# Performance work log

Hardware: AMD Instinct MI355X
Metric: run time of the kernel (lower is better)

## Reference

```python
import jax, jax.numpy as jnp
import numpy as np

S, B, IN, HID, DEPTH = 512, 64, 512, 512, 5
KEEP_IN = 1.0 - 0.75   # input_dropout = 0.75
KEEP_HID = 1.0 - 0.25  # hidden_dropout = 0.25


def _lin_init(k, shape, fan_in):
    bound = 1.0 / np.sqrt(fan_in)
    return jax.random.uniform(k, shape, jnp.float32, -bound, bound)


def setup_inputs() -> dict:
    key = jax.random.key(0)
    ks = jax.random.split(key, 14)
    inp = jax.random.normal(ks[0], (S, B, IN), jnp.float32)
    hidden = jax.random.normal(ks[1], (B, HID), jnp.float32)
    # tied_noise=True -> one input mask shared by H/T/C, one hidden mask shared
    h_mask = jax.random.bernoulli(ks[2], KEEP_IN, (B, IN)).astype(jnp.float32) / KEEP_IN
    s_h_mask = jax.random.bernoulli(ks[3], KEEP_HID, (B, HID)).astype(jnp.float32) / KEEP_HID
    # input projections (torch nn.Linear: W [out,in], y = x W^T + b)
    Wih = _lin_init(ks[4], (HID, IN), IN)
    bih = _lin_init(ks[5], (HID,), IN)
    Wit = _lin_init(ks[6], (HID, IN), IN)
    bit = _lin_init(ks[7], (HID,), IN)
    Wic = _lin_init(ks[8], (HID, IN), IN)
    bic = _lin_init(ks[9], (HID,), IN)
    # recurrent depth layers; layer 0 has no bias (set to 0)
    Wh = _lin_init(ks[10], (DEPTH, HID, HID), HID)
    bh = _lin_init(ks[11], (DEPTH, HID), HID).at[0].set(0.0)
    Wt = _lin_init(ks[12], (DEPTH, HID, HID), HID)
    bt = _lin_init(ks[13], (DEPTH, HID), HID).at[0].set(0.0)
    return dict(inp=inp, hidden=hidden, h_mask=h_mask, s_h_mask=s_h_mask,
                Wih=Wih, bih=bih, Wit=Wit, bit=bit, Wic=Wic, bic=bic,
                Wh=Wh, bh=bh, Wt=Wt, bt=bt)


def reference(inp, hidden, h_mask, s_h_mask, Wih, bih, Wit, bit, Wic, bic, Wh, bh, Wt, bt):
    # masked input (tied noise: same mask for H/T/C)
    mx = h_mask[None, :, :] * inp                      # [S,B,IN]
    H = jnp.einsum('sbi,hi->sbh', mx, Wih) + bih       # [S,B,HID]
    T = jnp.einsum('sbi,hi->sbh', mx, Wit) + bit
    C = jnp.einsum('sbi,hi->sbh', mx, Wic) + bic

    def step(s, htc):
        H_t, T_t, C_t = htc
        for l in range(DEPTH):
            sm = s_h_mask * s                          # [B,HID]
            lin_h = sm @ Wh[l].T + bh[l]
            lin_t = sm @ Wt[l].T + bt[l]               # NOTE: original uses rnn_t for C gate too
            if l == 0:
                h = jnp.tanh(H_t + lin_h)
                t = jax.nn.sigmoid(T_t + lin_t)
                c = jax.nn.sigmoid(C_t + lin_t)
            else:
                h = jnp.tanh(lin_h)
                t = jax.nn.sigmoid(lin_t)
                c = jax.nn.sigmoid(lin_t)
            s = h * t + s * c
        return s, s

    last, outs = jax.lax.scan(step, hidden, (H, T, C))
    return outs, last
```

## Files before the change

### kernel.cpp

```cpp
#include <hip/hip_runtime.h>
#include <math.h>

#define S_LEN 512
#define BATCH 64
#define IN_DIM 512
#define HID 512
#define DEPTH 5
#define N3 1536

typedef float floatx4 __attribute__((ext_vector_type(4)));
typedef unsigned int uintx4 __attribute__((ext_vector_type(4)));

__global__ __launch_bounds__(256) void rhn_inproj(
    const float* __restrict__ inp, const float* __restrict__ h_mask,
    const float* __restrict__ Wih, const float* __restrict__ Wit,
    const float* __restrict__ Wic, const float* __restrict__ bih,
    const float* __restrict__ bit_, const float* __restrict__ bic,
    float* __restrict__ HTC)
{
    constexpr int BM = 128, BN = 128, BK = 16, LW = BM + 4;
    __shared__ float As[BK][LW];
    __shared__ float Bs[BK][LW];
    const int m0 = blockIdx.x * BM;
    const int n0 = blockIdx.y * BN;
    const int tid = threadIdx.x;
    const int lrow = tid & 127;
    const int lkq  = tid >> 7;
    const int tx = tid & 15, ty = tid >> 4;

    const float* Arow = inp + (size_t)(m0 + lrow) * 512;
    const float* Mrow = h_mask + (size_t)((m0 + lrow) & 63) * 512;
    const int n = n0 + lrow;
    const float* Wrow = (n < 512) ? (Wih + (size_t)n * 512)
                       : (n < 1024) ? (Wit + (size_t)(n - 512) * 512)
                                    : (Wic + (size_t)(n - 1024) * 512);

    float acc[8][8] = {};

    for (int k0 = 0; k0 < 512; k0 += BK) {
#pragma unroll
        for (int it = 0; it < 2; ++it) {
            int kq = lkq * 2 + it;
            float4 av = *(const float4*)(Arow + k0 + kq * 4);
            float4 mv = *(const float4*)(Mrow + k0 + kq * 4);
            float4 bv = *(const float4*)(Wrow + k0 + kq * 4);
            As[kq * 4 + 0][lrow] = av.x * mv.x;
            As[kq * 4 + 1][lrow] = av.y * mv.y;
            As[kq * 4 + 2][lrow] = av.z * mv.z;
            As[kq * 4 + 3][lrow] = av.w * mv.w;
            Bs[kq * 4 + 0][lrow] = bv.x;
            Bs[kq * 4 + 1][lrow] = bv.y;
            Bs[kq * 4 + 2][lrow] = bv.z;
            Bs[kq * 4 + 3][lrow] = bv.w;
        }
        __syncthreads();
#pragma unroll
        for (int kk = 0; kk < BK; ++kk) {
            float4 a0 = *(const float4*)&As[kk][ty * 8];
            float4 a1 = *(const float4*)&As[kk][ty * 8 + 4];
            float4 bv0 = *(const float4*)&Bs[kk][tx * 8];
            float4 bv1 = *(const float4*)&Bs[kk][tx * 8 + 4];
            float am[8] = {a0.x, a0.y, a0.z, a0.w, a1.x, a1.y, a1.z, a1.w};
            float bn[8] = {bv0.x, bv0.y, bv0.z, bv0.w, bv1.x, bv1.y, bv1.z, bv1.w};
#pragma unroll
            for (int i = 0; i < 8; ++i)
#pragma unroll
                for (int j = 0; j < 8; ++j)
                    acc[i][j] += am[i] * bn[j];
        }
        __syncthreads();
    }

    float bias[8];
#pragma unroll
    for (int j = 0; j < 8; ++j) {
        int nn = n0 + tx * 8 + j;
        bias[j] = (nn < 512) ? bih[nn] : (nn < 1024) ? bit_[nn - 512] : bic[nn - 1024];
    }
#pragma unroll
    for (int i = 0; i < 8; ++i) {
        int mm = m0 + ty * 8 + i;
        float4 o0, o1;
        o0.x = acc[i][0] + bias[0]; o0.y = acc[i][1] + bias[1];
        o0.z = acc[i][2] + bias[2]; o0.w = acc[i][3] + bias[3];
        o1.x = acc[i][4] + bias[4]; o1.y = acc[i][5] + bias[5];
        o1.z = acc[i][6] + bias[6]; o1.w = acc[i][7] + bias[7];
        *(float4*)(HTC + (size_t)mm * N3 + n0 + tx * 8)     = o0;
        *(float4*)(HTC + (size_t)mm * N3 + n0 + tx * 8 + 4) = o1;
    }
}

__device__ __forceinline__ float fast_sig(float x) {
    return __builtin_amdgcn_rcpf(1.f + __expf(-x));
}
__device__ __forceinline__ float fast_tanh(float x) {
    return 2.f * fast_sig(2.f * x) - 1.f;
}

__global__ __launch_bounds__(512, 2) void rhn_scan(
    const float* __restrict__ hidden,
    const float* __restrict__ s_h_mask,
    const float* __restrict__ Wh, const float* __restrict__ bh,
    const float* __restrict__ Wt, const float* __restrict__ bt,
    const float* __restrict__ HTC,
    float* __restrict__ exch,
    float* __restrict__ out)
{
    __shared__ float sm_s[8][HID];
    __shared__ float linT[16][8];

    const int tid  = threadIdx.x;
    const int lane = tid & 63;
    const int w    = tid >> 6;
    const int c    = lane & 3;
    const int kq   = (lane >> 2) & 15;
    const int gh   = w * 4 + c;
    const int g    = gh >> 4;
    const int hl   = gh & 15;

    const int hi = blockIdx.x >> 3;
    const int bi = blockIdx.x & 7;
    const int h0 = hi * 16, b0 = bi * 8;

    const int myb = ((kq & 1) << 2) | (kq & 2) | ((kq >> 2) & 1);
    const bool own = (g == 0) && (kq < 8);
    const bool lw  = (g == 1) && (kq < 8);

    const float* Wsrc = g ? Wt : Wh;
    float4 Wreg[DEPTH * 8];
#pragma unroll
    for (int l = 0; l < DEPTH; ++l)
#pragma unroll
        for (int j = 0; j < 8; ++j)
            Wreg[l * 8 + j] = *(const float4*)(Wsrc
                + ((size_t)l * HID + (h0 + hl)) * HID + (size_t)(j * 16 + kq) * 4);

    float biasr[DEPTH];
    const float* bsrc = g ? bt : bh;
#pragma unroll
    for (int l = 0; l < DEPTH; ++l) biasr[l] = bsrc[l * HID + h0 + hl];

    const int pA = tid,       pB = tid + 512;
    const int bA = pA >> 7,   kA = pA & 127;
    const int bB = pB >> 7,   kB = pB & 127;
    const size_t offA = ((size_t)(b0 + bA) * HID + (size_t)kA * 4) * sizeof(float);
    const size_t offB = ((size_t)(b0 + bB) * HID + (size_t)kB * 4) * sizeof(float);
    const size_t SLOT = (size_t)BATCH * HID * sizeof(float);

    float s = 0.f, mymask = 0.f, Hp = 0.f, Tp = 0.f, Cp = 0.f;
    size_t ownoff = 0;
    if (own) {
        const int gb = b0 + myb, hh = h0 + hl;
        s      = hidden[(size_t)gb * HID + hh];
        mymask = s_h_mask[(size_t)gb * HID + hh];
        const float* hp = HTC + (size_t)gb * N3 + hh;
        Hp = hp[0]; Tp = hp[512]; Cp = hp[1024];
        ownoff = ((size_t)gb * HID + hh) * sizeof(float);
        unsigned uu = (__float_as_uint(s * mymask) & ~7u);
        char* p = (char*)exch + ownoff;
        asm volatile("global_store_dword %0, %1, off sc1" :: "v"(p), "v"(uu) : "memory");
    }

    const float4* smq = (const float4*)&sm_s[0][0] + kq;

    int seq = 0;
    for (int step = 0; step < S_LEN; ++step) {
#define ROUND(L)                                                                  \
        {                                                                         \
            const unsigned tg = (unsigned)(seq & 7);                              \
            const char* sb = (const char*)exch + (size_t)(seq & 1) * SLOT;        \
            const char* pa = sb + offA;                                           \
            const char* pb = sb + offB;                                           \
            uintx4 ua, ub;                                                        \
            for (;;) {                                                            \
                asm volatile("global_load_dwordx4 %0, %2, off sc1\n\t"            \
                             "global_load_dwordx4 %1, %3, off sc1\n\t"            \
                             "s_waitcnt vmcnt(0)"                                 \
                             : "=&v"(ua), "=&v"(ub)                               \
                             : "v"(pa), "v"(pb) : "memory");                      \
                unsigned mm = (ua.x ^ tg) | (ua.y ^ tg) | (ua.z ^ tg) | (ua.w ^ tg) \
                            | (ub.x ^ tg) | (ub.y ^ tg) | (ub.z ^ tg) | (ub.w ^ tg); \
                if ((mm & 7u) == 0u) break;                                       \
            }                                                                     \
            *(uintx4*)&sm_s[bA][kA * 4] = ua;                                     \
            *(uintx4*)&sm_s[bB][kB * 4] = ub;                                     \
            __syncthreads();                         \
            float acc[8] = {0.f, 0.f, 0.f, 0.f, 0.f, 0.f, 0.f, 0.f};              \
            _Pragma("unroll")                                                     \
            for (int j = 0; j < 8; ++j) {                                         \
                const float4 wv = Wreg[(L) * 8 + j];                              \
                _Pragma("unroll")                                                 \
                for (int b = 0; b < 8; ++b) {                                     \
                    const float4 sv = smq[b * 128 + j * 16];                      \
                    acc[b] = fmaf(wv.x, sv.x, acc[b]);                            \
                    acc[b] = fmaf(wv.y, sv.y, acc[b]);                            \
                    acc[b] = fmaf(wv.z, sv.z, acc[b]);                            \
                    acc[b] = fmaf(wv.w, sv.w, acc[b]);                            \
                }                                                                 \
            }                                                                     \
            {           \
                const bool u0 = (lane & 4) != 0;                                  \
                const bool u1 = (lane & 8) != 0;                                  \
                const bool u2 = (lane & 16) != 0;                                 \
                _Pragma("unroll")                                                 \
                for (int i = 0; i < 4; ++i) {                                     \
                    float snd = u0 ? acc[i] : acc[i + 4];                         \
                    float kp  = u0 ? acc[i + 4] : acc[i];                         \
                    acc[i] = kp + __shfl_xor(snd, 4);                             \
                }                                                                 \
                _Pragma("unroll")                                                 \
                for (int i = 0; i < 2; ++i) {                                     \
                    float snd = u1 ? acc[i] : acc[i + 2];                         \
                    float kp  = u1 ? acc[i + 2] : acc[i];                         \
                    acc[i] = kp + __shfl_xor(snd, 8);                             \
                }                                                                 \
                {                                                                 \
                    float snd = u2 ? acc[0] : acc[1];                             \
                    float kp  = u2 ? acc[1] : acc[0];                             \
                    acc[0] = kp + __shfl_xor(snd, 16);                            \
                }                                                                 \
                acc[0] += __shfl_xor(acc[0], 32);                                 \
            }                                                                     \
            const float lin = acc[0] + biasr[L];                                  \
            if (lw) linT[hl][myb] = lin;                                          \
            __syncthreads();                \
            if (own) {                                                            \
                const float lt = linT[hl][myb];                                   \
                float hv, tv, cv;                                                 \
                if ((L) == 0) {                                                   \
                    hv = fast_tanh(Hp + lin);                                     \
                    tv = fast_sig(Tp + lt);                                       \
                    cv = fast_sig(Cp + lt);                                       \
                } else {                                                          \
                    hv = fast_tanh(lin);                                          \
                    tv = fast_sig(lt);                                            \
                    cv = tv;                                                      \
                }                                                                 \
                s = hv * tv + s * cv;                                             \
                unsigned uu = (__float_as_uint(s * mymask) & ~7u)                 \
                            | (unsigned)((seq + 1) & 7);                          \
                char* p = (char*)exch + (size_t)((seq + 1) & 1) * SLOT + ownoff;  \
                asm volatile("global_store_dword %0, %1, off sc1"                 \
                             :: "v"(p), "v"(uu) : "memory");                      \
                if ((L) == 0 && step + 1 < S_LEN) {                               \
                    const float* hp = HTC + ((size_t)(step + 1) * BATCH           \
                                      + (b0 + myb)) * N3 + (h0 + hl);             \
                    Hp = hp[0]; Tp = hp[512]; Cp = hp[1024];                      \
                }                                                                 \
                if ((L) == DEPTH - 1)                                             \
                    out[((size_t)step * BATCH + (b0 + myb)) * HID + (h0 + hl)] = s; \
            }                                                                     \
            ++seq;                                                                \
        }
        ROUND(0) ROUND(1) ROUND(2) ROUND(3) ROUND(4)
#undef ROUND
    }

    if (own)
        out[(size_t)S_LEN * BATCH * HID + (size_t)(b0 + myb) * HID + (h0 + hl)] = s;
}

extern "C" void kernel_launch(void* const* d_in, const int* in_sizes, int n_in,
                              void* d_out, int out_size, void* d_ws, size_t ws_size,
                              hipStream_t stream) {
    const float* inp      = (const float*)d_in[0];
    const float* hidden   = (const float*)d_in[1];
    const float* h_mask   = (const float*)d_in[2];
    const float* s_h_mask = (const float*)d_in[3];
    const float* Wih = (const float*)d_in[4];
    const float* bih = (const float*)d_in[5];
    const float* Wit = (const float*)d_in[6];
    const float* bit_ = (const float*)d_in[7];
    const float* Wic = (const float*)d_in[8];
    const float* bic = (const float*)d_in[9];
    const float* Wh = (const float*)d_in[10];
    const float* bh = (const float*)d_in[11];
    const float* Wt = (const float*)d_in[12];
    const float* bt = (const float*)d_in[13];
    float* out = (float*)d_out;

    float* HTC  = (float*)d_ws;
    float* exch = HTC + (size_t)32768 * N3;

    (void)hipMemsetAsync(exch, 0xFF, 2 * (size_t)BATCH * HID * sizeof(float), stream);

    dim3 g1(256, 12);
    rhn_inproj<<<g1, 256, 0, stream>>>(inp, h_mask, Wih, Wit, Wic, bih, bit_, bic, HTC);

    void* args[] = {(void*)&hidden, (void*)&s_h_mask, (void*)&Wh, (void*)&bh,
                    (void*)&Wt, (void*)&bt, (void*)&HTC, (void*)&exch, (void*)&out};
    (void)hipLaunchCooperativeKernel((void*)rhn_scan, dim3(256), dim3(512), args, 0, stream);
}
```

Baseline: 17.37 ms.

## Replace tagged-payload polling with per-wave flag counters for inter-block sync

Blocks stop encoding a 3-bit sequence tag in the low bits of each exchanged value. Each of the 4 owner waves now publishes a monotonically increasing counter flag after its stores drain. Readers spin on one flag dword before issuing a single payload load, instead of repeatedly reloading two dwordx4 payloads. This cuts polling traffic and keeps full-precision values, but adds a vmcnt wait plus a flag store per round and relies on store ordering between the payload and the flag.

```diff
diff --git a/kernel.cpp b/kernel.cpp
--- a/kernel.cpp
+++ b/kernel.cpp
@@ -104,6 +104,7 @@
     const float* __restrict__ Wt, const float* __restrict__ bt,
     const float* __restrict__ HTC,
     float* __restrict__ exch,
+    unsigned* __restrict__ flags,
     float* __restrict__ out)
 {
     __shared__ float sm_s[8][HID];
@@ -140,12 +141,14 @@
 #pragma unroll
     for (int l = 0; l < DEPTH; ++l) biasr[l] = bsrc[l * HID + h0 + hl];
 
-    const int pA = tid,       pB = tid + 512;
-    const int bA = pA >> 7,   kA = pA & 127;
-    const int bB = pB >> 7,   kB = pB & 127;
+    const int bA = tid >> 7,  kA = tid & 127;
+    const int bB = bA + 4,    kB = kA;
     const size_t offA = ((size_t)(b0 + bA) * HID + (size_t)kA * 4) * sizeof(float);
     const size_t offB = ((size_t)(b0 + bB) * HID + (size_t)kB * 4) * sizeof(float);
     const size_t SLOT = (size_t)BATCH * HID * sizeof(float);
+
+    const unsigned* fp = flags + (((size_t)bi * 32 + (kA >> 2)) * 4 + (kA & 3));
+    unsigned* fme = flags + (((size_t)bi * 32 + hi) * 4 + w);
 
     float s = 0.f, mymask = 0.f, Hp = 0.f, Tp = 0.f, Cp = 0.f;
     size_t ownoff = 0;
@@ -156,9 +159,17 @@
         const float* hp = HTC + (size_t)gb * N3 + hh;
         Hp = hp[0]; Tp = hp[512]; Cp = hp[1024];
         ownoff = ((size_t)gb * HID + hh) * sizeof(float);
-        unsigned uu = (__float_as_uint(s * mymask) & ~7u);
+        float v = s * mymask;
         char* p = (char*)exch + ownoff;
-        asm volatile("global_store_dword %0, %1, off sc1" :: "v"(p), "v"(uu) : "memory");
+        asm volatile("global_store_dword %0, %1, off sc1" :: "v"(p), "v"(v) : "memory");
+    }
+    if (w < 4) {
+        asm volatile("s_waitcnt vmcnt(0)" ::: "memory");
+        if (lane == 0) {
+            unsigned one = 1u;
+            asm volatile("global_store_dword %0, %1, off sc1"
+                         :: "v"(fme), "v"(one) : "memory");
+        }
     }
 
     const float4* smq = (const float4*)&sm_s[0][0] + kq;
@@ -167,21 +178,23 @@
     for (int step = 0; step < S_LEN; ++step) {
 #define ROUND(L)                                                                  \
         {                                                                         \
-            const unsigned tg = (unsigned)(seq & 7);                              \
+            const unsigned target = (unsigned)(seq + 1);                          \
             const char* sb = (const char*)exch + (size_t)(seq & 1) * SLOT;        \
             const char* pa = sb + offA;                                           \
             const char* pb = sb + offB;                                           \
+            unsigned fv;                                                          \
+            for (;;) {                                                            \
+                asm volatile("global_load_dword %0, %1, off sc1\n\t"              \
+                             "s_waitcnt vmcnt(0)"                                 \
+                             : "=v"(fv) : "v"(fp) : "memory");                    \
+                if (fv >= target) break;                                          \
+            }                                                                     \
             uintx4 ua, ub;                                                        \
-            for (;;) {                                                            \
-                asm volatile("global_load_dwordx4 %0, %2, off sc1\n\t"            \
-                             "global_load_dwordx4 %1, %3, off sc1\n\t"            \
-                             "s_waitcnt vmcnt(0)"                                 \
-                             : "=&v"(ua), "=&v"(ub)                               \
-                             : "v"(pa), "v"(pb) : "memory");                      \
-                unsigned mm = (ua.x ^ tg) | (ua.y ^ tg) | (ua.z ^ tg) | (ua.w ^ tg) \
-                            | (ub.x ^ tg) | (ub.y ^ tg) | (ub.z ^ tg) | (ub.w ^ tg); \
-                if ((mm & 7u) == 0u) break;                                       \
-            }                                                                     \
+            asm volatile("global_load_dwordx4 %0, %2, off sc1\n\t"                \
+                         "global_load_dwordx4 %1, %3, off sc1\n\t"                \
+                         "s_waitcnt vmcnt(0)"                                     \
+                         : "=&v"(ua), "=&v"(ub)                                   \
+                         : "v"(pa), "v"(pb) : "memory");                          \
             *(uintx4*)&sm_s[bA][kA * 4] = ua;                                     \
             *(uintx4*)&sm_s[bB][kB * 4] = ub;                                     \
             __syncthreads();                         \
@@ -237,18 +250,27 @@
                     cv = tv;                                                      \
                 }                                                                 \
                 s = hv * tv + s * cv;                                             \
-                unsigned uu = (__float_as_uint(s * mymask) & ~7u)                 \
-                            | (unsigned)((seq + 1) & 7);                          \
+                float v = s * mymask;                                             \
                 char* p = (char*)exch + (size_t)((seq + 1) & 1) * SLOT + ownoff;  \
                 asm volatile("global_store_dword %0, %1, off sc1"                 \
-                             :: "v"(p), "v"(uu) : "memory");                      \
+                             :: "v"(p), "v"(v) : "memory");                       \
+            }                                                                     \
+            if (w < 4) {      \
+                asm volatile("s_waitcnt vmcnt(0)" ::: "memory");                  \
+                if (lane == 0) {                                                  \
+                    unsigned nf = (unsigned)(seq + 2);                            \
+                    asm volatile("global_store_dword %0, %1, off sc1"             \
+                                 :: "v"(fme), "v"(nf) : "memory");                \
+                }                                                                 \
+            }                                                                     \
+            if (own) {           \
+                if ((L) == DEPTH - 1)                                             \
+                    out[((size_t)step * BATCH + (b0 + myb)) * HID + (h0 + hl)] = s; \
                 if ((L) == 0 && step + 1 < S_LEN) {                               \
                     const float* hp = HTC + ((size_t)(step + 1) * BATCH           \
                                       + (b0 + myb)) * N3 + (h0 + hl);             \
                     Hp = hp[0]; Tp = hp[512]; Cp = hp[1024];                      \
                 }                                                                 \
-                if ((L) == DEPTH - 1)                                             \
-                    out[((size_t)step * BATCH + (b0 + myb)) * HID + (h0 + hl)] = s; \
             }                                                                     \
             ++seq;                                                                \
         }
@@ -281,13 +303,15 @@
 
     float* HTC  = (float*)d_ws;
     float* exch = HTC + (size_t)32768 * N3;
-
-    (void)hipMemsetAsync(exch, 0xFF, 2 * (size_t)BATCH * HID * sizeof(float), stream);
+    unsigned* flags = (unsigned*)(exch + 2 * (size_t)BATCH * HID);
+
+    (void)hipMemsetAsync(flags, 0, 8 * 32 * 4 * sizeof(unsigned), stream);
 
     dim3 g1(256, 12);
     rhn_inproj<<<g1, 256, 0, stream>>>(inp, h_mask, Wih, Wit, Wic, bih, bit_, bic, HTC);
 
     void* args[] = {(void*)&hidden, (void*)&s_h_mask, (void*)&Wh, (void*)&bh,
-                    (void*)&Wt, (void*)&bt, (void*)&HTC, (void*)&exch, (void*)&out};
+                    (void*)&Wt, (void*)&bt, (void*)&HTC, (void*)&exch,
+                    (void*)&flags, (void*)&out};
     (void)hipLaunchCooperativeKernel((void*)rhn_scan, dim3(256), dim3(512), args, 0, stream);
 }
```

Result: slower. 25.87 ms (+48.9%).

## Add fast local-scope exchange buffer with fallback to system-coherent polling

Applied to the files above, without the earlier changes.

Each owner thread now writes its state to two exchange buffers: one stored with sc0 (narrower coherence scope) and one with sc1. Consumers first poll the sc0 copy a bounded number of times and switch permanently to the sc1 copy if the tagged values never appear. Polling loops gain s_sleep back-off and an iteration budget. The intent is cheaper cross-block handoff per depth round, at the cost of doubled stores and possible stale reads across XCDs, which would cause fallback or, once the budget runs out, silently wrong data.

```diff
diff --git a/kernel.cpp b/kernel.cpp
--- a/kernel.cpp
+++ b/kernel.cpp
@@ -7,6 +7,7 @@
 #define HID 512
 #define DEPTH 5
 #define N3 1536
+#define NBLK 256
 
 typedef float floatx4 __attribute__((ext_vector_type(4)));
 typedef unsigned int uintx4 __attribute__((ext_vector_type(4)));
@@ -103,7 +104,8 @@
     const float* __restrict__ Wh, const float* __restrict__ bh,
     const float* __restrict__ Wt, const float* __restrict__ bt,
     const float* __restrict__ HTC,
-    float* __restrict__ exch,
+    float* __restrict__ exch_g,
+    float* __restrict__ exch_l,
     float* __restrict__ out)
 {
     __shared__ float sm_s[8][HID];
@@ -140,9 +142,8 @@
 #pragma unroll
     for (int l = 0; l < DEPTH; ++l) biasr[l] = bsrc[l * HID + h0 + hl];
 
-    const int pA = tid,       pB = tid + 512;
-    const int bA = pA >> 7,   kA = pA & 127;
-    const int bB = pB >> 7,   kB = pB & 127;
+    const int bA = tid >> 7,  kA = tid & 127;
+    const int bB = bA + 4,    kB = kA;
     const size_t offA = ((size_t)(b0 + bA) * HID + (size_t)kA * 4) * sizeof(float);
     const size_t offB = ((size_t)(b0 + bB) * HID + (size_t)kB * 4) * sizeof(float);
     const size_t SLOT = (size_t)BATCH * HID * sizeof(float);
@@ -157,30 +158,58 @@
         Hp = hp[0]; Tp = hp[512]; Cp = hp[1024];
         ownoff = ((size_t)gb * HID + hh) * sizeof(float);
         unsigned uu = (__float_as_uint(s * mymask) & ~7u);
-        char* p = (char*)exch + ownoff;
-        asm volatile("global_store_dword %0, %1, off sc1" :: "v"(p), "v"(uu) : "memory");
+        char* pl = (char*)exch_l + ownoff;
+        char* pg = (char*)exch_g + ownoff;
+        asm volatile("global_store_dword %0, %1, off sc0" :: "v"(pl), "v"(uu) : "memory");
+        asm volatile("global_store_dword %0, %1, off sc1" :: "v"(pg), "v"(uu) : "memory");
     }
 
     const float4* smq = (const float4*)&sm_s[0][0] + kq;
 
+    bool st1 = false;
+    int budget = 1 << 23;
     int seq = 0;
     for (int step = 0; step < S_LEN; ++step) {
 #define ROUND(L)                                                                  \
         {                                                                         \
             const unsigned tg = (unsigned)(seq & 7);                              \
-            const char* sb = (const char*)exch + (size_t)(seq & 1) * SLOT;        \
-            const char* pa = sb + offA;                                           \
-            const char* pb = sb + offB;                                           \
+            const size_t sbo = (size_t)(seq & 1) * SLOT;                          \
             uintx4 ua, ub;                                                        \
-            for (;;) {                                                            \
-                asm volatile("global_load_dwordx4 %0, %2, off sc1\n\t"            \
-                             "global_load_dwordx4 %1, %3, off sc1\n\t"            \
-                             "s_waitcnt vmcnt(0)"                                 \
-                             : "=&v"(ua), "=&v"(ub)                               \
-                             : "v"(pa), "v"(pb) : "memory");                      \
-                unsigned mm = (ua.x ^ tg) | (ua.y ^ tg) | (ua.z ^ tg) | (ua.w ^ tg) \
-                            | (ub.x ^ tg) | (ub.y ^ tg) | (ub.z ^ tg) | (ub.w ^ tg); \
-                if ((mm & 7u) == 0u) break;                                       \
+            bool got = false;                                                     \
+            if (!st1) {       \
+                const char* pal = (const char*)exch_l + sbo + offA;               \
+                const char* pbl = (const char*)exch_l + sbo + offB;               \
+                _Pragma("unroll 1")                                               \
+                for (int it = 0; it < 48; ++it) {                                 \
+                    asm volatile("global_load_dwordx4 %0, %2, off sc0\n\t"        \
+                                 "global_load_dwordx4 %1, %3, off sc0\n\t"        \
+                                 "s_waitcnt vmcnt(0)"                             \
+                                 : "=&v"(ua), "=&v"(ub)                           \
+                                 : "v"(pal), "v"(pbl) : "memory");                \
+                    unsigned m = ((ua.x ^ tg) | (ua.y ^ tg) | (ua.z ^ tg)         \
+                                | (ua.w ^ tg) | (ub.x ^ tg) | (ub.y ^ tg)         \
+                                | (ub.z ^ tg) | (ub.w ^ tg)) & 7u;                \
+                    if (m == 0u) { got = true; break; }                           \
+                    __builtin_amdgcn_s_sleep(1);                                  \
+                }                                                                 \
+                if (!got) st1 = true;                                             \
+            }                                                                     \
+            if (!got) {        \
+                const char* pag = (const char*)exch_g + sbo + offA;               \
+                const char* pbg = (const char*)exch_g + sbo + offB;               \
+                _Pragma("unroll 1")                                               \
+                do {                                                              \
+                    asm volatile("global_load_dwordx4 %0, %2, off sc1\n\t"        \
+                                 "global_load_dwordx4 %1, %3, off sc1\n\t"        \
+                                 "s_waitcnt vmcnt(0)"                             \
+                                 : "=&v"(ua), "=&v"(ub)                           \
+                                 : "v"(pag), "v"(pbg) : "memory");                \
+                    unsigned m = ((ua.x ^ tg) | (ua.y ^ tg) | (ua.z ^ tg)         \
+                                | (ua.w ^ tg) | (ub.x ^ tg) | (ub.y ^ tg)         \
+                                | (ub.z ^ tg) | (ub.w ^ tg)) & 7u;                \
+                    if (m == 0u) break;                                           \
+                    __builtin_amdgcn_s_sleep(1);                                  \
+                } while (--budget > 0);                                           \
             }                                                                     \
             *(uintx4*)&sm_s[bA][kA * 4] = ua;                                     \
             *(uintx4*)&sm_s[bB][kB * 4] = ub;                                     \
@@ -223,7 +252,7 @@
             }                                                                     \
             const float lin = acc[0] + biasr[L];                                  \
             if (lw) linT[hl][myb] = lin;                                          \
-            __syncthreads();                \
+            __syncthreads();            \
             if (own) {                                                            \
                 const float lt = linT[hl][myb];                                   \
                 float hv, tv, cv;                                                 \
@@ -239,16 +268,20 @@
                 s = hv * tv + s * cv;                                             \
                 unsigned uu = (__float_as_uint(s * mymask) & ~7u)                 \
                             | (unsigned)((seq + 1) & 7);                          \
-                char* p = (char*)exch + (size_t)((seq + 1) & 1) * SLOT + ownoff;  \
+                const size_t po = (size_t)((seq + 1) & 1) * SLOT + ownoff;        \
+                char* pl = (char*)exch_l + po;                                    \
+                char* pg = (char*)exch_g + po;                                    \
+                asm volatile("global_store_dword %0, %1, off sc0"                 \
+                             :: "v"(pl), "v"(uu) : "memory");                     \
                 asm volatile("global_store_dword %0, %1, off sc1"                 \
-                             :: "v"(p), "v"(uu) : "memory");                      \
-                if ((L) == 0 && step + 1 < S_LEN) {                               \
-                    const float* hp = HTC + ((size_t)(step + 1) * BATCH           \
-                                      + (b0 + myb)) * N3 + (h0 + hl);             \
-                    Hp = hp[0]; Tp = hp[512]; Cp = hp[1024];                      \
-                }                                                                 \
+                             :: "v"(pg), "v"(uu) : "memory");                     \
                 if ((L) == DEPTH - 1)                                             \
                     out[((size_t)step * BATCH + (b0 + myb)) * HID + (h0 + hl)] = s; \
+                if ((L) == 0 && step + 1 < S_LEN) {                               \
+                    const float* hp = HTC + ((size_t)((step + 1) * BATCH          \
+                                      + (b0 + myb))) * N3 + (h0 + hl);            \
+                    Hp = hp[0]; Tp = hp[512]; Cp = hp[1024];                      \
+                }                                                                 \
             }                                                                     \
             ++seq;                                                                \
         }
@@ -279,15 +312,17 @@
     const float* bt = (const float*)d_in[13];
     float* out = (float*)d_out;
 
-    float* HTC  = (float*)d_ws;
-    float* exch = HTC + (size_t)32768 * N3;
-
-    (void)hipMemsetAsync(exch, 0xFF, 2 * (size_t)BATCH * HID * sizeof(float), stream);
+    float* HTC    = (float*)d_ws;
+    float* exch_g = HTC + (size_t)32768 * N3;
+    float* exch_l = exch_g + 2 * (size_t)BATCH * HID;
+
+    (void)hipMemsetAsync(exch_g, 0xFF, 4 * (size_t)BATCH * HID * sizeof(float), stream);
 
     dim3 g1(256, 12);
     rhn_inproj<<<g1, 256, 0, stream>>>(inp, h_mask, Wih, Wit, Wic, bih, bit_, bic, HTC);
 
     void* args[] = {(void*)&hidden, (void*)&s_h_mask, (void*)&Wh, (void*)&bh,
-                    (void*)&Wt, (void*)&bt, (void*)&HTC, (void*)&exch, (void*)&out};
-    (void)hipLaunchCooperativeKernel((void*)rhn_scan, dim3(256), dim3(512), args, 0, stream);
-}
+                    (void*)&Wt, (void*)&bt, (void*)&HTC, (void*)&exch_g,
+                    (void*)&exch_l, (void*)&out};
+    (void)hipLaunchCooperativeKernel((void*)rhn_scan, dim3(NBLK), dim3(512), args, 0, stream);
+}
```

Measured after the change: 19.00 ms. 9.4% more time.
